# Kernel optimization log

Measured on AMD Instinct MI355X. Metric: run time of the kernel, lower is better.

Reference implementation:

```python
import jax, jax.numpy as jnp
import numpy as np

HEAD_DIM = 64  # init arg `dim`; scale divisor is sqrt(dim)


def setup_inputs() -> dict:
    key = jax.random.key(0)
    k1, k2 = jax.random.split(key)
    x1 = jax.random.normal(k1, (16, 2048, 64), dtype=jnp.float32)
    x2 = jax.random.normal(k2, (16, 2048, 64), dtype=jnp.float32)
    return {"x1": x1, "x2": x2}


def reference(x1, x2):
    # qk: [B, Sq, Sk]
    qk = jnp.einsum("bqd,bkd->bqk", x1, x2)
    inv_scale = jnp.sqrt(jnp.asarray(HEAD_DIM, dtype=x1.dtype))
    attn = jax.nn.softmax(qk / inv_scale, axis=-1)
    # dropout is identity in eval / p=0
    out = jnp.einsum("bqk,bkd->bqd", attn, x2)
    return out
```

## Files before the change

### kernel.cpp

```cpp
#include <hip/hip_runtime.h>
#include <hip/hip_bf16.h>


typedef __attribute__((ext_vector_type(8))) short short8;
typedef __attribute__((ext_vector_type(16))) float f32x16;

#define MFMA32(a, b, c) __builtin_amdgcn_mfma_f32_32x32x16_bf16(a, b, c, 0, 0, 0)

union frag_u { short8 s8; unsigned u[4]; };

static __device__ __forceinline__ unsigned pk2(float a, float b) {
    __hip_bfloat162 h = __float22bfloat162_rn(float2{a, b});
    union { __hip_bfloat162 h2; unsigned u; } cv;
    cv.h2 = h;
    return cv.u;
}

static __device__ __forceinline__ unsigned cvtpk(float a, float b) {
    unsigned r;
    asm("v_cvt_pk_bf16_f32 %0, %1, %2" : "=v"(r) : "v"(a), "v"(b));
    return r;
}

static __device__ __forceinline__ short8 cvt8(const float* p, float sc) {
    float4 a = *(const float4*)p;
    float4 b = *(const float4*)(p + 4);
    frag_u f;
    f.u[0] = pk2(a.x * sc, a.y * sc);
    f.u[1] = pk2(a.z * sc, a.w * sc);
    f.u[2] = pk2(b.x * sc, b.y * sc);
    f.u[3] = pk2(b.z * sc, b.w * sc);
    return f.s8;
}

static __device__ __forceinline__ void pl32swap(unsigned& a, unsigned& b) {
    asm("v_permlane32_swap_b32 %0, %1" : "+v"(a), "+v"(b));
}

__global__ __launch_bounds__(256) void prep_kernel(
    const float* __restrict__ x2, short* __restrict__ kf, short* __restrict__ vf)
{
    int idx = blockIdx.x * 256 + threadIdx.x;
    int chunk = idx >> 6;
    int l = idx & 63;
    int lo = l & 31, hi = l >> 5;
    int c = chunk & 4095;
    int b = c >> 8;
    int kt = (c >> 2) & 63;
    if (chunk < 4096) {
        int ds = c & 3;
        const float* src = x2 + ((size_t)(b * 2048 + kt * 32 + lo)) * 64 + ds * 16 + 8 * hi;
        ((short8*)kf)[(size_t)c * 64 + l] = cvt8(src, 1.0f);
    } else {
        int ks = (c >> 1) & 1;
        int dc = c & 1;
        const float* base = x2 + ((size_t)(b * 2048 + kt * 32 + ks * 16 + 8 * hi)) * 64 + dc * 32 + lo;
        frag_u o;
#pragma unroll
        for (int jj = 0; jj < 4; ++jj)
            o.u[jj] = pk2(base[(2 * jj) * 64], base[(2 * jj + 1) * 64]);
        ((short8*)vf)[(size_t)c * 64 + l] = o.s8;
    }
}

__global__ __launch_bounds__(512) void attn_kernel(
    const float* __restrict__ x1,
    const short* __restrict__ kf, const short* __restrict__ vf,
    float* __restrict__ out)
{
    __shared__ short8 sbuf[2][32][64];
    __shared__ float  ldl[2][4][64];

    const int l  = threadIdx.x & 63;
    const int w  = threadIdx.x >> 6;
    const int lo = l & 31, hi = l >> 5;
    const int qsel = w & 1;
    const int ks   = w >> 1;

    const int bid = blockIdx.x;
    const int wi  = bid >> 3;
    const int b   = (bid & 7) * 2 + (wi >> 5);
    const int qg  = wi & 31;
    const int qt  = qg * 2 + qsel;
    const int qrow = qt * 32 + lo;
    const size_t bbase = (size_t)b * 2048 * 64;

    const float QSC = 0.125f * 1.4426950408889634f;
    short8 qf[4];
    const float* qp = x1 + bbase + (size_t)qrow * 64 + 8 * hi;
#pragma unroll
    for (int ds = 0; ds < 4; ++ds) qf[ds] = cvt8(qp + ds * 16, QSC);

    f32x16 oacc0, oacc1;
#pragma unroll
    for (int r = 0; r < 16; ++r) { oacc0[r] = 0.f; oacc1[r] = 0.f; }
    float lsum = 0.f;

    const int cc0 = qsel * 4;
    const short8* g_src = (qsel == 0 ? (const short8*)kf : (const short8*)vf)
                        + ((size_t)((b * 64 + ks * 16) * 4)) * 64 + l;

    short8 st0 = g_src[0], st1 = g_src[64], st2 = g_src[128], st3 = g_src[192];
    sbuf[0][ks * 8 + cc0 + 0][l] = st0;
    sbuf[0][ks * 8 + cc0 + 1][l] = st1;
    sbuf[0][ks * 8 + cc0 + 2][l] = st2;
    sbuf[0][ks * 8 + cc0 + 3][l] = st3;
    __syncthreads();

#pragma unroll 2
    for (int t = 0; t < 16; ++t) {
        const int cur = t & 1, nxt = cur ^ 1;

        if (t < 15) {
            const short8* gs = g_src + (size_t)(t + 1) * 256;
            st0 = gs[0]; st1 = gs[64]; st2 = gs[128]; st3 = gs[192];
        }

        short8 k0 = sbuf[cur][ks * 8 + 0][l];
        short8 k1 = sbuf[cur][ks * 8 + 1][l];
        short8 k2 = sbuf[cur][ks * 8 + 2][l];
        short8 k3 = sbuf[cur][ks * 8 + 3][l];
        f32x16 s;
#pragma unroll
        for (int r = 0; r < 16; ++r) s[r] = 0.f;
        __builtin_amdgcn_s_setprio(1);
        s = MFMA32(k0, qf[0], s);
        s = MFMA32(k1, qf[1], s);
        s = MFMA32(k2, qf[2], s);
        s = MFMA32(k3, qf[3], s);
        __builtin_amdgcn_s_setprio(0);

        unsigned pw[8];
        float rs = 0.f;
#pragma unroll
        for (int i = 0; i < 8; ++i) {
            float pa = __builtin_amdgcn_exp2f(s[2 * i]);
            float pb = __builtin_amdgcn_exp2f(s[2 * i + 1]);
            rs += pa + pb;
            pw[i] = cvtpk(pa, pb);
        }
        lsum += rs;

        pl32swap(pw[0], pw[2]);
        pl32swap(pw[1], pw[3]);
        pl32swap(pw[4], pw[6]);
        pl32swap(pw[5], pw[7]);
        frag_u pb0, pb1;
        pb0.u[0] = pw[0]; pb0.u[1] = pw[1]; pb0.u[2] = pw[2]; pb0.u[3] = pw[3];
        pb1.u[0] = pw[4]; pb1.u[1] = pw[5]; pb1.u[2] = pw[6]; pb1.u[3] = pw[7];

        short8 v0 = sbuf[cur][ks * 8 + 4][l];
        short8 v1 = sbuf[cur][ks * 8 + 5][l];
        short8 v2 = sbuf[cur][ks * 8 + 6][l];
        short8 v3 = sbuf[cur][ks * 8 + 7][l];
        __builtin_amdgcn_s_setprio(1);
        oacc0 = MFMA32(v0, pb0.s8, oacc0);
        oacc1 = MFMA32(v1, pb0.s8, oacc1);
        oacc0 = MFMA32(v2, pb1.s8, oacc0);
        oacc1 = MFMA32(v3, pb1.s8, oacc1);
        __builtin_amdgcn_s_setprio(0);

        if (t < 15) {
            sbuf[nxt][ks * 8 + cc0 + 0][l] = st0;
            sbuf[nxt][ks * 8 + cc0 + 1][l] = st1;
            sbuf[nxt][ks * 8 + cc0 + 2][l] = st2;
            sbuf[nxt][ks * 8 + cc0 + 3][l] = st3;
        }
        __syncthreads();
    }

    float* red = (float*)&sbuf[0][0][0];
    ldl[qsel][ks][l] = lsum;
    float* myred = red + ((size_t)((qsel * 4 + ks) * 32)) * 64 + l;
#pragma unroll
    for (int r = 0; r < 16; ++r) {
        myred[r * 64]        = oacc0[r];
        myred[(16 + r) * 64] = oacc1[r];
    }
    __syncthreads();

    float lt = 0.f;
#pragma unroll
    for (int s4 = 0; s4 < 4; ++s4) lt += ldl[qsel][s4][lo] + ldl[qsel][s4][lo + 32];
    float inv = 1.0f / lt;

    float* op = out + bbase + (size_t)qrow * 64;
#pragma unroll
    for (int i = 0; i < 8; ++i) {
        int rr = ks * 8 + i;
        float v = red[((qsel * 4 + 0) * 32 + rr) * 64 + l]
                + red[((qsel * 4 + 1) * 32 + rr) * 64 + l]
                + red[((qsel * 4 + 2) * 32 + rr) * 64 + l]
                + red[((qsel * 4 + 3) * 32 + rr) * 64 + l];
        int r = rr & 15;
        int d = (r & 3) + 8 * (r >> 2) + 4 * hi + 32 * (rr >> 4);
        op[d] = v * inv;
    }
}

extern "C" void kernel_launch(void* const* d_in, const int* in_sizes, int n_in,
                              void* d_out, int out_size, void* d_ws, size_t ws_size,
                              hipStream_t stream) {
    const float* x1 = (const float*)d_in[0];
    const float* x2 = (const float*)d_in[1];
    float* out = (float*)d_out;

    short* kf = (short*)d_ws;
    short* vf = kf + (size_t)4096 * 512;

    hipLaunchKernelGGL(prep_kernel, dim3(2048), dim3(256), 0, stream, x2, kf, vf);
    hipLaunchKernelGGL(attn_kernel, dim3(512), dim3(512), 0, stream, x1, kf, vf, out);
}
```

Baseline: 41.55 us.

## Stream K/V tiles directly into LDS with global_load_lds and two-deep prefetch

Replaces register-staged K/V loads (global load into VGPRs, then an LDS store) with direct global-to-LDS async loads through the global_load_lds builtin. Tile t+2 is issued into the freed buffer after a barrier, and explicit vmcnt waits plus split barriers keep two tiles in flight. The s_setprio hints around the MFMAs are removed. This aims to hide global latency and cut VGPR and LDS-store traffic, at the cost of an extra barrier per iteration and reliance on hand-placed waitcnt correctness.

```diff
diff --git a/kernel.cpp b/kernel.cpp
--- a/kernel.cpp
+++ b/kernel.cpp
@@ -68,7 +68,7 @@
     const short* __restrict__ kf, const short* __restrict__ vf,
     float* __restrict__ out)
 {
-    __shared__ short8 sbuf[2][32][64];
+    __shared__ short8 sbuf[2][4][8][64];
     __shared__ float  ldl[2][4][64];
 
     const int l  = threadIdx.x & 63;
@@ -97,38 +97,42 @@
     float lsum = 0.f;
 
     const int cc0 = qsel * 4;
-    const short8* g_src = (qsel == 0 ? (const short8*)kf : (const short8*)vf)
-                        + ((size_t)((b * 64 + ks * 16) * 4)) * 64 + l;
-
-    short8 st0 = g_src[0], st1 = g_src[64], st2 = g_src[128], st3 = g_src[192];
-    sbuf[0][ks * 8 + cc0 + 0][l] = st0;
-    sbuf[0][ks * 8 + cc0 + 1][l] = st1;
-    sbuf[0][ks * 8 + cc0 + 2][l] = st2;
-    sbuf[0][ks * 8 + cc0 + 3][l] = st3;
-    __syncthreads();
+    const char* gbase = (const char*)(qsel == 0 ? kf : vf)
+                      + ((size_t)((b * 64 + ks * 16) * 4)) * 1024 + (size_t)l * 16;
+
+#define STAGE(T, BUF)                                                          \
+    {                                                                          \
+        const char* g_ = gbase + (size_t)(T) * 4096;                           \
+        _Pragma("unroll")                                                      \
+        for (int i_ = 0; i_ < 4; ++i_) {                                       \
+            __builtin_amdgcn_global_load_lds(                                  \
+                (const __attribute__((address_space(1))) void*)(g_ + i_ * 1024),\
+                (__attribute__((address_space(3))) void*)&sbuf[BUF][ks][cc0 + i_][0], \
+                16, 0, 0);                                                     \
+        }                                                                      \
+    }
+
+    STAGE(0, 0);
+    STAGE(1, 1);
+    asm volatile("s_waitcnt vmcnt(4)" ::: "memory");
+    __builtin_amdgcn_sched_barrier(0);
+    __builtin_amdgcn_s_barrier();
 
 #pragma unroll 2
     for (int t = 0; t < 16; ++t) {
-        const int cur = t & 1, nxt = cur ^ 1;
-
-        if (t < 15) {
-            const short8* gs = g_src + (size_t)(t + 1) * 256;
-            st0 = gs[0]; st1 = gs[64]; st2 = gs[128]; st3 = gs[192];
-        }
-
-        short8 k0 = sbuf[cur][ks * 8 + 0][l];
-        short8 k1 = sbuf[cur][ks * 8 + 1][l];
-        short8 k2 = sbuf[cur][ks * 8 + 2][l];
-        short8 k3 = sbuf[cur][ks * 8 + 3][l];
+        const int cur = t & 1;
+
+        short8 k0 = sbuf[cur][ks][0][l];
+        short8 k1 = sbuf[cur][ks][1][l];
+        short8 k2 = sbuf[cur][ks][2][l];
+        short8 k3 = sbuf[cur][ks][3][l];
         f32x16 s;
 #pragma unroll
         for (int r = 0; r < 16; ++r) s[r] = 0.f;
-        __builtin_amdgcn_s_setprio(1);
         s = MFMA32(k0, qf[0], s);
         s = MFMA32(k1, qf[1], s);
         s = MFMA32(k2, qf[2], s);
         s = MFMA32(k3, qf[3], s);
-        __builtin_amdgcn_s_setprio(0);
 
         unsigned pw[8];
         float rs = 0.f;
@@ -149,27 +153,29 @@
         pb0.u[0] = pw[0]; pb0.u[1] = pw[1]; pb0.u[2] = pw[2]; pb0.u[3] = pw[3];
         pb1.u[0] = pw[4]; pb1.u[1] = pw[5]; pb1.u[2] = pw[6]; pb1.u[3] = pw[7];
 
-        short8 v0 = sbuf[cur][ks * 8 + 4][l];
-        short8 v1 = sbuf[cur][ks * 8 + 5][l];
-        short8 v2 = sbuf[cur][ks * 8 + 6][l];
-        short8 v3 = sbuf[cur][ks * 8 + 7][l];
-        __builtin_amdgcn_s_setprio(1);
+        short8 v0 = sbuf[cur][ks][4][l];
+        short8 v1 = sbuf[cur][ks][5][l];
+        short8 v2 = sbuf[cur][ks][6][l];
+        short8 v3 = sbuf[cur][ks][7][l];
         oacc0 = MFMA32(v0, pb0.s8, oacc0);
         oacc1 = MFMA32(v1, pb0.s8, oacc1);
         oacc0 = MFMA32(v2, pb1.s8, oacc0);
         oacc1 = MFMA32(v3, pb1.s8, oacc1);
-        __builtin_amdgcn_s_setprio(0);
-
-        if (t < 15) {
-            sbuf[nxt][ks * 8 + cc0 + 0][l] = st0;
-            sbuf[nxt][ks * 8 + cc0 + 1][l] = st1;
-            sbuf[nxt][ks * 8 + cc0 + 2][l] = st2;
-            sbuf[nxt][ks * 8 + cc0 + 3][l] = st3;
+
+        __builtin_amdgcn_s_barrier();
+        if (t + 2 < 16) {
+            STAGE(t + 2, cur);
+            asm volatile("s_waitcnt vmcnt(4)" ::: "memory");
+        } else {
+            asm volatile("s_waitcnt vmcnt(0)" ::: "memory");
         }
-        __syncthreads();
-    }
-
-    float* red = (float*)&sbuf[0][0][0];
+        __builtin_amdgcn_sched_barrier(0);
+        __builtin_amdgcn_s_barrier();
+    }
+
+#undef STAGE
+
+    float* red = (float*)&sbuf[0][0][0][0];
     ldl[qsel][ks][l] = lsum;
     float* myred = red + ((size_t)((qsel * 4 + ks) * 32)) * 64 + l;
 #pragma unroll
```

Measured after the change: 38.57 us. -7.2%, faster.
